# Performance work log

Measured on AMD Instinct MI355X. Metric: run time of the kernel, lower is better.

The kernel has to match this reference:

```python
import jax, jax.numpy as jnp
import numpy as np

B, W, H, C = 8, 32, 32, 64   # batch, width, height, hidden_size (per-head dim)
NH = 8                        # num_attention_heads
P = 64                        # position_encoding_size
M = 32                        # max_position_embeddings
AH = C * NH                   # all_head_size


def setup_inputs() -> dict:
    key = jax.random.key(0)
    ks = jax.random.split(key, 10)
    s = 0.02
    return {
        "hidden_states": jax.random.normal(ks[0], (B, W, H, C), jnp.float32),
        "attention_mask": jnp.zeros((B, W, H), jnp.float32),  # unused by forward (kept for signature parity)
        "row_emb": jax.random.normal(ks[1], (2 * M - 1, P), jnp.float32) * s,
        "col_emb": jax.random.normal(ks[2], (2 * M - 1, P), jnp.float32) * s,
        "w_row": jax.random.normal(ks[3], (NH, P), jnp.float32) * s,  # head_keys_row.weight (no bias)
        "w_col": jax.random.normal(ks[4], (NH, P), jnp.float32) * s,  # head_keys_col.weight (no bias)
        "w_q": jax.random.normal(ks[5], (AH, C), jnp.float32) * s,
        "b_q": jnp.zeros((AH,), jnp.float32),
        "w_k": jax.random.normal(ks[6], (AH, C), jnp.float32) * s,
        "b_k": jnp.zeros((AH,), jnp.float32),
        "w_v": jax.random.normal(ks[7], (C, AH), jnp.float32) * s,  # value: Linear(all_head_size, hidden_size)
        "b_v": jnp.zeros((C,), jnp.float32),
    }


def reference(hidden_states, attention_mask, row_emb, col_emb, w_row, w_col,
              w_q, b_q, w_k, b_k, w_v, b_v):
    b, w, h, c = hidden_states.shape
    nh = w_row.shape[0]
    # relative index table (buffer)
    rel = (jnp.arange(M)[None, :] - jnp.arange(M)[:, None]) + (M - 1)  # (M, M)

    # positional scores
    ri_w = rel[:w, :w].reshape(-1)                                   # (w*w,)
    row_scores = (row_emb[ri_w] @ w_row.T).reshape(1, w, 1, w, nh)   # axis pattern: j,l
    ri_h = rel[:h, :h].reshape(-1)
    col_scores = (col_emb[ri_h] @ w_col.T).reshape(h, 1, h, 1, nh)   # axis pattern: i,k
    pos = (row_scores + col_scores).transpose(0, 1, 4, 2, 3)         # (h, w, nh, h, w)

    # data-dependent scores (use_attention_data=True)
    q = (hidden_states @ w_q.T + b_q).reshape(b, w, h, nh, c)
    k = (hidden_states @ w_k.T + b_k).reshape(b, w, h, nh, c)
    data = jnp.einsum('bijhd,bklhd->bijhkl', q, k) / jnp.sqrt(jnp.float32(c))

    scores = pos[None] + data                                        # (b, w, h, nh, w, h)  (w==h)
    probs = jax.nn.softmax(scores.reshape(b, h, w, nh, h * w), axis=-1)
    probs = probs.reshape(b, h, w, nh, h, w)

    out = jnp.einsum('bijhkl,bkld->bijhd', probs, hidden_states)     # (b, w, h, nh, c)
    out = out.reshape(b, w, h, nh * c)
    return out @ w_v.T + b_v
```

## Files before the change

kernel.cpp:

```cpp
#include <hip/hip_runtime.h>
#include <hip/hip_bf16.h>
#include <cstdint>
#include <cstddef>

#define SB 8
#define SNH 8
#define SS 1024
#define SC 64

typedef __attribute__((ext_vector_type(8)))  short bf16x8;
typedef __attribute__((ext_vector_type(4)))  short bf16x4;
typedef __attribute__((ext_vector_type(4)))  float f32x4;
typedef __attribute__((ext_vector_type(16))) float f32x16;
typedef __attribute__((ext_vector_type(4)))  unsigned u32x4;

#define INVLN2 1.44269504088896f
#define QSCALE (0.125f * INVLN2)

static __device__ __forceinline__ short f2bf(float f) {
    __hip_bfloat16 h = __float2bfloat16(f);
    return __builtin_bit_cast(short, h);
}
static __device__ __forceinline__ float bf2f(short s) {
    return __builtin_bit_cast(float, (unsigned)((unsigned short)s) << 16);
}

static __device__ __forceinline__ bf16x8 cvt8(const float* __restrict__ p, float scl) {
    const float4 a = *(const float4*)p;
    const float4 b = *(const float4*)(p + 4);
    bf16x8 o;
    o[0] = f2bf(a.x * scl); o[1] = f2bf(a.y * scl); o[2] = f2bf(a.z * scl); o[3] = f2bf(a.w * scl);
    o[4] = f2bf(b.x * scl); o[5] = f2bf(b.y * scl); o[6] = f2bf(b.z * scl); o[7] = f2bf(b.w * scl);
    return o;
}
static __device__ __forceinline__ bf16x8 cvt8v(float4 a, float4 b) {
    bf16x8 o;
    o[0] = f2bf(a.x); o[1] = f2bf(a.y); o[2] = f2bf(a.z); o[3] = f2bf(a.w);
    o[4] = f2bf(b.x); o[5] = f2bf(b.y); o[6] = f2bf(b.z); o[7] = f2bf(b.w);
    return o;
}

static __device__ __forceinline__ unsigned pk2(float lo, float hi) {
    return (unsigned)(unsigned short)f2bf(lo) | ((unsigned)(unsigned short)f2bf(hi) << 16);
}

#if __has_builtin(__builtin_amdgcn_permlane32_swap)
typedef __attribute__((ext_vector_type(2))) unsigned uint2v;
static __device__ __forceinline__ void plswap(unsigned& a, unsigned& b) {
    uint2v r = __builtin_amdgcn_permlane32_swap(a, b, false, false);
    a = r[0]; b = r[1];
}
#else
static __device__ __forceinline__ void plswap(unsigned& a, unsigned& b) {
    asm volatile("v_permlane32_swap_b32 %0, %1" : "+v"(a), "+v"(b));
}
#endif

static __device__ __forceinline__ float xhalf_sum(float x) {
    unsigned a = __builtin_bit_cast(unsigned, x), b = a;
    plswap(a, b);
    return __builtin_bit_cast(float, a) + __builtin_bit_cast(float, b);
}

#define MFMA32(a, b, c) __builtin_amdgcn_mfma_f32_32x32x16_bf16((a), (b), (c), 0, 0, 0)

static __device__ __forceinline__ void dlayout_to_bfrag(const float* src, bf16x8* dst) {
#pragma unroll
    for (int k = 0; k < 4; ++k) {
        const int base = (k >> 1) * 16 + (k & 1) * 8;
        unsigned w0 = pk2(src[base + 0], src[base + 1]);
        unsigned w2 = pk2(src[base + 4], src[base + 5]);
        plswap(w0, w2);
        unsigned w1 = pk2(src[base + 2], src[base + 3]);
        unsigned w3 = pk2(src[base + 6], src[base + 7]);
        plswap(w1, w3);
        u32x4 uw; uw[0] = w0; uw[1] = w1; uw[2] = w2; uw[3] = w3;
        dst[k] = __builtin_bit_cast(bf16x8, uw);
    }
}

static __device__ __forceinline__ void dhalf_to_bfrag(const float* src, bf16x8* dst) {
#pragma unroll
    for (int k = 0; k < 2; ++k) {
        const int base = k * 8;
        unsigned w0 = pk2(src[base + 0], src[base + 1]);
        unsigned w2 = pk2(src[base + 4], src[base + 5]);
        plswap(w0, w2);
        unsigned w1 = pk2(src[base + 2], src[base + 3]);
        unsigned w3 = pk2(src[base + 6], src[base + 7]);
        plswap(w1, w3);
        u32x4 uw; uw[0] = w0; uw[1] = w1; uw[2] = w2; uw[3] = w3;
        dst[k] = __builtin_bit_cast(bf16x8, uw);
    }
}

__global__ __launch_bounds__(256) void prep1(
    const float* __restrict__ row_emb, const float* __restrict__ col_emb,
    const float* __restrict__ w_row,   const float* __restrict__ w_col,
    const float* __restrict__ w_v,  const float* __restrict__ w_q,
    const float* __restrict__ w_k,  const float* __restrict__ hid,
    const float* __restrict__ b_q,  const float* __restrict__ b_k,
    float* __restrict__ posRow, float* __restrict__ posCol,
    short* __restrict__ wvB, short* __restrict__ hidB, short* __restrict__ VtBw,
    short* __restrict__ MqBt, float* __restrict__ row0,
    float* __restrict__ vn, float* __restrict__ snv)
{
    const int bx = blockIdx.x;
    const int tid = threadIdx.x;
    __shared__ float T[64][65];

    if (bx < 64) {
        const int idx = bx * 256 + tid;
        const int which = idx >> 13;
        const int r = idx & 8191;
        const int n = r >> 10;
        const int j = (r >> 5) & 31;
        const int l = r & 31;
        const float* emb = which ? col_emb : row_emb;
        const float* wgt = which ? w_col : w_row;
        const int e = l - j + 31;
        float acc = 0.f;
        for (int p = 0; p < 64; p += 4) {
            const float4 ev = *(const float4*)&emb[e * 64 + p];
            const float4 wv4 = *(const float4*)&wgt[n * 64 + p];
            acc += ev.x * wv4.x + ev.y * wv4.y + ev.z * wv4.z + ev.w * wv4.w;
        }
        (which ? posCol : posRow)[r] = acc * INVLN2;
    } else if (bx < 80) {
        const int t = (bx - 64) * 256 + tid;
        *(bf16x8*)&wvB[t * 8] = cvt8(&w_v[t * 8], 1.0f);
    } else if (bx < 208) {
        const int z = bx - 80;
        const int b = z & 7, kt = z >> 3;
        const int r  = tid >> 2;
        const int c0 = (tid & 3) * 16;
        const float* src = hid + (((size_t)b * 1024) + kt * 64 + r) * 64 + c0;
        const float4 f0 = ((const float4*)src)[0];
        const float4 f1 = ((const float4*)src)[1];
        const float4 f2 = ((const float4*)src)[2];
        const float4 f3 = ((const float4*)src)[3];
        T[r][c0 + 0] = f0.x; T[r][c0 + 1] = f0.y; T[r][c0 + 2] = f0.z; T[r][c0 + 3] = f0.w;
        T[r][c0 + 4] = f1.x; T[r][c0 + 5] = f1.y; T[r][c0 + 6] = f1.z; T[r][c0 + 7] = f1.w;
        T[r][c0 + 8] = f2.x; T[r][c0 + 9] = f2.y; T[r][c0 +10] = f2.z; T[r][c0 +11] = f2.w;
        T[r][c0 +12] = f3.x; T[r][c0 +13] = f3.y; T[r][c0 +14] = f3.z; T[r][c0 +15] = f3.w;
        short* hb = hidB + (((size_t)b * 1024) + kt * 64 + r) * 64 + c0;
        *(bf16x8*)(hb)     = cvt8v(f0, f1);
        *(bf16x8*)(hb + 8) = cvt8v(f2, f3);
        __syncthreads();
        short* tbase = VtBw + ((size_t)(b * 16 + kt)) * 4096;
#pragma unroll
        for (int it = 0; it < 2; ++it) {
            const int d  = (tid >> 3) + 32 * it;
            const int k0 = (tid & 7) * 8;
            bf16x8 o;
#pragma unroll
            for (int j = 0; j < 8; ++j) o[j] = f2bf(T[k0 + j][d]);
            *(bf16x8*)&tbase[d * 64 + k0] = o;
        }
    } else {
        const int n = bx - 208;
        const int wv = tid >> 6;
        const int lane = tid & 63;
        if (wv == 0) {
            const int h = lane >> 5, qc = lane & 31;
            bf16x8 afr[2][4], bfr[2][4];
#pragma unroll
            for (int ct = 0; ct < 2; ++ct)
#pragma unroll
                for (int k = 0; k < 4; ++k) {
                    bf16x8 oa, ob;
#pragma unroll
                    for (int j = 0; j < 8; ++j) {
                        const int a = 16 * k + 8 * h + j;
                        oa[j] = f2bf(w_q[(size_t)(n * 64 + a) * 64 + 32 * ct + qc] * QSCALE);
                        ob[j] = f2bf(w_k[(size_t)(n * 64 + a) * 64 + 32 * ct + qc]);
                    }
                    afr[ct][k] = oa; bfr[ct][k] = ob;
                }
#pragma unroll
            for (int ct1 = 0; ct1 < 2; ++ct1)
#pragma unroll
                for (int ctc = 0; ctc < 2; ++ctc) {
                    f32x16 d;
#pragma unroll
                    for (int i = 0; i < 16; ++i) d[i] = 0.f;
                    d = MFMA32(afr[ct1][0], bfr[ctc][0], d);
                    d = MFMA32(afr[ct1][1], bfr[ctc][1], d);
                    d = MFMA32(afr[ct1][2], bfr[ctc][2], d);
                    d = MFMA32(afr[ct1][3], bfr[ctc][3], d);
                    short* mb = MqBt + n * 4096 + (32 * ctc + qc) * 64 + 32 * ct1 + 4 * h;
#pragma unroll
                    for (int rg = 0; rg < 4; ++rg) {
                        bf16x4 ov;
                        ov[0] = f2bf(d[4 * rg + 0]); ov[1] = f2bf(d[4 * rg + 1]);
                        ov[2] = f2bf(d[4 * rg + 2]); ov[3] = f2bf(d[4 * rg + 3]);
                        *(bf16x4*)&mb[8 * rg] = ov;
                    }
                }
        } else if (wv == 1) {
            const int c2 = lane;
            float acc = 0.f;
            for (int a = 0; a < 64; ++a)
                acc += b_q[n * 64 + a] * w_k[(size_t)(n * 64 + a) * 64 + c2];
            row0[n * 64 + c2] = acc * QSCALE;
        } else if (wv == 2) {
            const int c1 = lane;
            float acc = 0.f;
            for (int a = 0; a < 64; ++a)
                acc += b_k[n * 64 + a] * w_q[(size_t)(n * 64 + a) * 64 + c1];
            vn[n * 64 + c1] = acc * QSCALE;
        } else {
            float p = b_q[n * 64 + lane] * b_k[n * 64 + lane];
#pragma unroll
            for (int o = 1; o < 64; o <<= 1) p += __shfl_xor(p, o);
            if (lane == 0) snv[n] = p * QSCALE;
        }
    }
}

__global__ __launch_bounds__(512, 1) void attn_fused(
    const short* __restrict__ hidB, const short* __restrict__ VtBw,
    const short* __restrict__ MqBt, const float* __restrict__ row0,
    const float* __restrict__ vn,   const float* __restrict__ snv,
    const float* __restrict__ posRow, const float* __restrict__ posCol,
    const short* __restrict__ wvB, const float* __restrict__ bv,
    float* __restrict__ out)
{
    const int orig = blockIdx.x;
    const int swzb = (orig & 7) * 32 + (orig >> 3);
    const int b    = swzb >> 5;
    const int qt   = swzb & 31;

    const int tid  = threadIdx.x;
    const int w    = tid >> 6;
    const int n    = w;
    const int lane = tid & 63;
    const int h    = lane >> 5;
    const int qc   = lane & 31;
    const int q    = qt * 32 + qc;
    const int swz  = qc & 7;

    __shared__ __align__(16) short lds[32768];
    short* const Kst0 = lds;
    short* const Vst0 = lds + 4096;
    short* const Kst1 = lds + 8192;
    short* const Vst1 = lds + 12288;

    bf16x8 qf[4];
    float cq;
    {
        const short* hrow = hidB + (((size_t)b * 1024) + q) * 64 + 8 * h;
        bf16x8 hq[4];
#pragma unroll
        for (int kk = 0; kk < 4; ++kk) hq[kk] = *(const bf16x8*)(hrow + 16 * kk);

        float aD[32];
#pragma unroll
        for (int ct = 0; ct < 2; ++ct) {
            f32x16 ci;
            const float* r0p = row0 + n * 64 + 32 * ct + 4 * h;
#pragma unroll
            for (int rg = 0; rg < 4; ++rg) {
                const float4 v = *(const float4*)(r0p + 8 * rg);
                ci[4 * rg + 0] = v.x; ci[4 * rg + 1] = v.y;
                ci[4 * rg + 2] = v.z; ci[4 * rg + 3] = v.w;
            }
            const short* mbase = MqBt + n * 4096 + (size_t)(32 * ct + qc) * 64 + 8 * h;
            ci = MFMA32(*(const bf16x8*)(mbase),      hq[0], ci);
            ci = MFMA32(*(const bf16x8*)(mbase + 16), hq[1], ci);
            ci = MFMA32(*(const bf16x8*)(mbase + 32), hq[2], ci);
            ci = MFMA32(*(const bf16x8*)(mbase + 48), hq[3], ci);
#pragma unroll
            for (int i = 0; i < 16; ++i) aD[16 * ct + i] = ci[i];
        }
        dlayout_to_bfrag(aD, qf);

        float part = 0.f;
#pragma unroll
        for (int kk = 0; kk < 4; ++kk) {
            const float4 v0 = *(const float4*)&vn[n * 64 + 16 * kk + 8 * h];
            const float4 v1 = *(const float4*)&vn[n * 64 + 16 * kk + 8 * h + 4];
            part += bf2f(hq[kk][0]) * v0.x + bf2f(hq[kk][1]) * v0.y +
                    bf2f(hq[kk][2]) * v0.z + bf2f(hq[kk][3]) * v0.w +
                    bf2f(hq[kk][4]) * v1.x + bf2f(hq[kk][5]) * v1.y +
                    bf2f(hq[kk][6]) * v1.z + bf2f(hq[kk][7]) * v1.w;
        }
        cq = xhalf_sum(part) + snv[n];
    }

    float prowA[16];
    {
        const float* pr = posRow + (n * 32 + qc) * 32 + 4 * h;
#pragma unroll
        for (int rg = 0; rg < 4; ++rg) {
            const float4 v = *(const float4*)(pr + 8 * rg);
            prowA[4 * rg + 0] = v.x + cq; prowA[4 * rg + 1] = v.y + cq;
            prowA[4 * rg + 2] = v.z + cq; prowA[4 * rg + 3] = v.w + cq;
        }
    }
    const float* pcp = posCol + (n * 32 + qt) * 32;

    const short* Kbase = hidB + (size_t)b * 65536;
    const short* Vbase = VtBw + (size_t)b * 65536;

    const int c16  = tid & 7;
    const int srow = tid >> 3;
    const int woff = srow * 128 + ((c16 ^ (srow & 7)) << 4);
    const short* kp = Kbase + (size_t)srow * 64 + c16 * 8;
    const short* vp = Vbase + (size_t)srow * 64 + c16 * 8;

    float lsum = 0.f;
    f32x16 oacc[2];
#pragma unroll
    for (int dt = 0; dt < 2; ++dt)
#pragma unroll
        for (int i = 0; i < 16; ++i) oacc[dt][i] = 0.f;

    auto compute = [&](int kt, const short* Ktc_s, const short* Vtc_s) {
        const char* Ktc = (const char*)Ktc_s;
        const char* Vtc = (const char*)Vtc_s;
        const float pcv[2] = {pcp[2 * kt], pcp[2 * kt + 1]};

        bf16x8 pfrag[4];
#pragma unroll
        for (int ct = 0; ct < 2; ++ct) {
            bf16x8 kf[4];
            const int rb = (32 * ct + qc) * 128;
#pragma unroll
            for (int k = 0; k < 4; ++k)
                kf[k] = *(const bf16x8*)(Ktc + rb + (((2 * k + h) ^ swz) << 4));

            f32x16 ci;
#pragma unroll
            for (int i = 0; i < 16; ++i) ci[i] = prowA[i] + pcv[ct];
            ci = MFMA32(kf[0], qf[0], ci);
            ci = MFMA32(kf[1], qf[1], ci);
            ci = MFMA32(kf[2], qf[2], ci);
            ci = MFMA32(kf[3], qf[3], ci);

            float p[16];
#pragma unroll
            for (int i = 0; i < 16; ++i) p[i] = __builtin_amdgcn_exp2f(ci[i]);
            float s8[8];
#pragma unroll
            for (int i = 0; i < 8; ++i) s8[i] = p[i] + p[i + 8];
            lsum += ((s8[0] + s8[1]) + (s8[2] + s8[3])) +
                    ((s8[4] + s8[5]) + (s8[6] + s8[7]));
            dhalf_to_bfrag(p, &pfrag[2 * ct]);
        }

        bf16x8 vf[2][4];
#pragma unroll
        for (int dt = 0; dt < 2; ++dt) {
            const int rb = (32 * dt + qc) * 128;
#pragma unroll
            for (int ks = 0; ks < 4; ++ks)
                vf[dt][ks] = *(const bf16x8*)(Vtc + rb + (((2 * ks + h) ^ swz) << 4));
        }
#pragma unroll
        for (int dt = 0; dt < 2; ++dt) {
            f32x16 oa = oacc[dt];
            oa = MFMA32(vf[dt][0], pfrag[0], oa);
            oa = MFMA32(vf[dt][1], pfrag[1], oa);
            oa = MFMA32(vf[dt][2], pfrag[2], oa);
            oacc[dt] = MFMA32(vf[dt][3], pfrag[3], oa);
        }
    };

    {
        const float4 a0 = *(const float4*)kp;
        const float4 a1 = *(const float4*)vp;
        *(float4*)((char*)Kst0 + woff) = a0;
        *(float4*)((char*)Vst0 + woff) = a1;
    }
    __syncthreads();

#pragma unroll 1
    for (int pr = 0; pr < 8; ++pr) {
        const int j0 = 2 * pr, j1 = j0 + 1;
        {
            const size_t o = (size_t)(j0 + 1) * 4096;
            const float4 a0 = *(const float4*)(kp + o);
            const float4 a1 = *(const float4*)(vp + o);
            compute(j0, Kst0, Vst0);
            *(float4*)((char*)Kst1 + woff) = a0;
            *(float4*)((char*)Vst1 + woff) = a1;
            __syncthreads();
        }
        if (j1 < 15) {
            const size_t o = (size_t)(j1 + 1) * 4096;
            const float4 a0 = *(const float4*)(kp + o);
            const float4 a1 = *(const float4*)(vp + o);
            compute(j1, Kst1, Vst1);
            *(float4*)((char*)Kst0 + woff) = a0;
            *(float4*)((char*)Vst0 + woff) = a1;
            __syncthreads();
        } else {
            compute(j1, Kst1, Vst1);
        }
    }

    const float inv = 1.0f / xhalf_sum(lsum);
    float hoD[32];
#pragma unroll
    for (int dt = 0; dt < 2; ++dt)
#pragma unroll
        for (int i = 0; i < 16; ++i) hoD[16 * dt + i] = oacc[dt][i] * inv;
    bf16x8 hofrag[4];
    dlayout_to_bfrag(hoD, hofrag);

    f32x16 dvacc[2];
#pragma unroll
    for (int ct = 0; ct < 2; ++ct)
#pragma unroll
        for (int i = 0; i < 16; ++i) dvacc[ct][i] = 0.f;
#pragma unroll
    for (int ct = 0; ct < 2; ++ct)
#pragma unroll
        for (int k = 0; k < 4; ++k) {
            const bf16x8 aw = *(const bf16x8*)&wvB[(size_t)(32 * ct + qc) * 512 +
                                                   n * 64 + 16 * k + 8 * h];
            dvacc[ct] = MFMA32(aw, hofrag[k], dvacc[ct]);
        }

    __syncthreads();
    float* cb = (float*)lds;
#pragma unroll
    for (int i = 0; i < 32; ++i)
        cb[n * 2048 + i * 64 + lane] = dvacc[i >> 4][i & 15];
    __syncthreads();

    float s[4];
#pragma unroll
    for (int k = 0; k < 4; ++k) {
        const int i = 4 * w + k;
        float acc = 0.f;
#pragma unroll
        for (int nn = 0; nn < 8; ++nn) acc += cb[nn * 2048 + i * 64 + lane];
        s[k] = acc;
    }
    const int dvb = 32 * (w >> 2) + 8 * (w & 3) + 4 * h;
    const float4 bb4 = *(const float4*)&bv[dvb];
    const int row = b * 1024 + qt * 32 + qc;
    *(float4*)&out[(size_t)row * 64 + dvb] =
        make_float4(s[0] + bb4.x, s[1] + bb4.y, s[2] + bb4.z, s[3] + bb4.w);
}

extern "C" void kernel_launch(void* const* d_in, const int* in_sizes, int n_in,
                              void* d_out, int out_size, void* d_ws, size_t ws_size,
                              hipStream_t stream)
{
    const float* hid     = (const float*)d_in[0];
    const float* row_emb = (const float*)d_in[2];
    const float* col_emb = (const float*)d_in[3];
    const float* w_row   = (const float*)d_in[4];
    const float* w_col   = (const float*)d_in[5];
    const float* w_q     = (const float*)d_in[6];
    const float* b_q     = (const float*)d_in[7];
    const float* w_k     = (const float*)d_in[8];
    const float* b_k     = (const float*)d_in[9];
    const float* w_v     = (const float*)d_in[10];
    const float* b_v     = (const float*)d_in[11];
    float* out = (float*)d_out;

    short* hidB   = (short*)d_ws;
    short* VtBw   = hidB + (size_t)SB * SS * SC;
    short* MqBt   = VtBw + (size_t)SB * SS * SC;
    float* posRow = (float*)(MqBt + SNH * SC * SC);
    float* posCol = posRow + SNH * 32 * 32;
    float* row0   = posCol + SNH * 32 * 32;
    float* vn     = row0 + SNH * SC;
    float* snv    = vn + SNH * SC;
    short* wvB    = (short*)(snv + 8);

    prep1<<<216, 256, 0, stream>>>(row_emb, col_emb, w_row, w_col, w_v, w_q,
                                   w_k, hid, b_q, b_k,
                                   posRow, posCol, wvB, hidB, VtBw,
                                   MqBt, row0, vn, snv);
    attn_fused<<<256, 512, 0, stream>>>(hidB, VtBw, MqBt, row0, vn, snv,
                                        posRow, posCol, wvB, b_v, out);
}
```

Measured before the change: 39.57 us.

## Split heads across two blocks and combine output projection with atomics

The attention kernel now launches 512 blocks of 256 threads, each handling four heads for one query tile, instead of 256 blocks of 512 threads covering all eight heads. The aim is more blocks and occupancy (two blocks per CU) on the GPU's many compute units. Each block reduces its four heads' partial value projections in shared memory and atomically adds them into the output. The prep kernel gains extra blocks that pre-initialise the output with the bias. This costs float atomics, output results that depend on the order of those atomics, and K/V tiles that are loaded twice per query tile.

```diff
diff --git a/kernel.cpp b/kernel.cpp
--- a/kernel.cpp
+++ b/kernel.cpp
@@ -100,10 +100,12 @@
     const float* __restrict__ w_v,  const float* __restrict__ w_q,
     const float* __restrict__ w_k,  const float* __restrict__ hid,
     const float* __restrict__ b_q,  const float* __restrict__ b_k,
+    const float* __restrict__ b_v,
     float* __restrict__ posRow, float* __restrict__ posCol,
     short* __restrict__ wvB, short* __restrict__ hidB, short* __restrict__ VtBw,
     short* __restrict__ MqBt, float* __restrict__ row0,
-    float* __restrict__ vn, float* __restrict__ snv)
+    float* __restrict__ vn, float* __restrict__ snv,
+    float* __restrict__ out)
 {
     const int bx = blockIdx.x;
     const int tid = threadIdx.x;
@@ -157,7 +159,7 @@
             for (int j = 0; j < 8; ++j) o[j] = f2bf(T[k0 + j][d]);
             *(bf16x8*)&tbase[d * 64 + k0] = o;
         }
-    } else {
+    } else if (bx < 216) {
         const int n = bx - 208;
         const int wv = tid >> 6;
         const int lane = tid & 63;
@@ -215,32 +217,45 @@
             for (int o = 1; o < 64; o <<= 1) p += __shfl_xor(p, o);
             if (lane == 0) snv[n] = p * QSCALE;
         }
-    }
-}
-
-__global__ __launch_bounds__(512, 1) void attn_fused(
+    } else {
+        const int t = (bx - 216) * 256 + tid;
+        float4 bvv[16];
+#pragma unroll
+        for (int i = 0; i < 16; ++i) bvv[i] = *(const float4*)&b_v[i * 4];
+#pragma unroll
+        for (int r = 0; r < 4; ++r) {
+            float* op = out + ((size_t)t * 4 + r) * 64;
+#pragma unroll
+            for (int i = 0; i < 16; ++i) *(float4*)&op[i * 4] = bvv[i];
+        }
+    }
+}
+
+__global__ __launch_bounds__(256, 2) void attn_fused(
     const short* __restrict__ hidB, const short* __restrict__ VtBw,
     const short* __restrict__ MqBt, const float* __restrict__ row0,
     const float* __restrict__ vn,   const float* __restrict__ snv,
     const float* __restrict__ posRow, const float* __restrict__ posCol,
-    const short* __restrict__ wvB, const float* __restrict__ bv,
+    const short* __restrict__ wvB,
     float* __restrict__ out)
 {
     const int orig = blockIdx.x;
-    const int swzb = (orig & 7) * 32 + (orig >> 3);
-    const int b    = swzb >> 5;
-    const int qt   = swzb & 31;
+    const int swzb = (orig & 7) * 64 + (orig >> 3);
+    const int b    = swzb >> 6;
+    const int rest = swzb & 63;
+    const int qt   = rest >> 1;
+    const int g    = rest & 1;
 
     const int tid  = threadIdx.x;
     const int w    = tid >> 6;
-    const int n    = w;
+    const int n    = g * 4 + w;
     const int lane = tid & 63;
     const int h    = lane >> 5;
     const int qc   = lane & 31;
     const int q    = qt * 32 + qc;
     const int swz  = qc & 7;
 
-    __shared__ __align__(16) short lds[32768];
+    __shared__ __align__(16) short lds[16384];
     short* const Kst0 = lds;
     short* const Vst0 = lds + 4096;
     short* const Kst1 = lds + 8192;
@@ -305,9 +320,12 @@
 
     const int c16  = tid & 7;
     const int srow = tid >> 3;
-    const int woff = srow * 128 + ((c16 ^ (srow & 7)) << 4);
-    const short* kp = Kbase + (size_t)srow * 64 + c16 * 8;
-    const short* vp = Vbase + (size_t)srow * 64 + c16 * 8;
+    const int woffA = srow * 128 + ((c16 ^ (srow & 7)) << 4);
+    const int woffB = (srow + 32) * 128 + ((c16 ^ (srow & 7)) << 4);
+    const short* kp0 = Kbase + (size_t)srow * 64 + c16 * 8;
+    const short* kp1 = Kbase + (size_t)(srow + 32) * 64 + c16 * 8;
+    const short* vp0 = Vbase + (size_t)srow * 64 + c16 * 8;
+    const short* vp1 = Vbase + (size_t)(srow + 32) * 64 + c16 * 8;
 
     float lsum = 0.f;
     f32x16 oacc[2];
@@ -368,35 +386,47 @@
     };
 
     {
-        const float4 a0 = *(const float4*)kp;
-        const float4 a1 = *(const float4*)vp;
-        *(float4*)((char*)Kst0 + woff) = a0;
-        *(float4*)((char*)Vst0 + woff) = a1;
+        const float4 a0 = *(const float4*)kp0;
+        const float4 a1 = *(const float4*)kp1;
+        const float4 a2 = *(const float4*)vp0;
+        const float4 a3 = *(const float4*)vp1;
+        *(float4*)((char*)Kst0 + woffA) = a0;
+        *(float4*)((char*)Kst0 + woffB) = a1;
+        *(float4*)((char*)Vst0 + woffA) = a2;
+        *(float4*)((char*)Vst0 + woffB) = a3;
     }
     __syncthreads();
 
 #pragma unroll 1
     for (int pr = 0; pr < 8; ++pr) {
-        const int j0 = 2 * pr, j1 = j0 + 1;
+        const int kt0 = 2 * pr, kt1 = kt0 + 1;
         {
-            const size_t o = (size_t)(j0 + 1) * 4096;
-            const float4 a0 = *(const float4*)(kp + o);
-            const float4 a1 = *(const float4*)(vp + o);
-            compute(j0, Kst0, Vst0);
-            *(float4*)((char*)Kst1 + woff) = a0;
-            *(float4*)((char*)Vst1 + woff) = a1;
+            const size_t o = (size_t)(kt0 + 1) * 4096;
+            const float4 a0 = *(const float4*)(kp0 + o);
+            const float4 a1 = *(const float4*)(kp1 + o);
+            const float4 a2 = *(const float4*)(vp0 + o);
+            const float4 a3 = *(const float4*)(vp1 + o);
+            compute(kt0, Kst0, Vst0);
+            *(float4*)((char*)Kst1 + woffA) = a0;
+            *(float4*)((char*)Kst1 + woffB) = a1;
+            *(float4*)((char*)Vst1 + woffA) = a2;
+            *(float4*)((char*)Vst1 + woffB) = a3;
             __syncthreads();
         }
-        if (j1 < 15) {
-            const size_t o = (size_t)(j1 + 1) * 4096;
-            const float4 a0 = *(const float4*)(kp + o);
-            const float4 a1 = *(const float4*)(vp + o);
-            compute(j1, Kst1, Vst1);
-            *(float4*)((char*)Kst0 + woff) = a0;
-            *(float4*)((char*)Vst0 + woff) = a1;
+        if (kt1 < 15) {
+            const size_t o = (size_t)(kt1 + 1) * 4096;
+            const float4 a0 = *(const float4*)(kp0 + o);
+            const float4 a1 = *(const float4*)(kp1 + o);
+            const float4 a2 = *(const float4*)(vp0 + o);
+            const float4 a3 = *(const float4*)(vp1 + o);
+            compute(kt1, Kst1, Vst1);
+            *(float4*)((char*)Kst0 + woffA) = a0;
+            *(float4*)((char*)Kst0 + woffB) = a1;
+            *(float4*)((char*)Vst0 + woffA) = a2;
+            *(float4*)((char*)Vst0 + woffB) = a3;
             __syncthreads();
         } else {
-            compute(j1, Kst1, Vst1);
+            compute(kt1, Kst1, Vst1);
         }
     }
 
@@ -427,23 +457,20 @@
     float* cb = (float*)lds;
 #pragma unroll
     for (int i = 0; i < 32; ++i)
-        cb[n * 2048 + i * 64 + lane] = dvacc[i >> 4][i & 15];
+        cb[w * 2048 + i * 64 + lane] = dvacc[i >> 4][i & 15];
     __syncthreads();
 
-    float s[4];
-#pragma unroll
-    for (int k = 0; k < 4; ++k) {
-        const int i = 4 * w + k;
-        float acc = 0.f;
-#pragma unroll
-        for (int nn = 0; nn < 8; ++nn) acc += cb[nn * 2048 + i * 64 + lane];
-        s[k] = acc;
-    }
-    const int dvb = 32 * (w >> 2) + 8 * (w & 3) + 4 * h;
-    const float4 bb4 = *(const float4*)&bv[dvb];
     const int row = b * 1024 + qt * 32 + qc;
-    *(float4*)&out[(size_t)row * 64 + dvb] =
-        make_float4(s[0] + bb4.x, s[1] + bb4.y, s[2] + bb4.z, s[3] + bb4.w);
+    float* orow = out + (size_t)row * 64;
+#pragma unroll
+    for (int k = 0; k < 8; ++k) {
+        const int i = 8 * w + k;
+        float acc = cb[i * 64 + lane];
+#pragma unroll
+        for (int nn = 1; nn < 4; ++nn) acc += cb[nn * 2048 + i * 64 + lane];
+        const int dv = 32 * (i >> 4) + 8 * ((i >> 2) & 3) + 4 * h + (i & 3);
+        atomicAdd(&orow[dv], acc);
+    }
 }
 
 extern "C" void kernel_launch(void* const* d_in, const int* in_sizes, int n_in,
@@ -473,10 +500,10 @@
     float* snv    = vn + SNH * SC;
     short* wvB    = (short*)(snv + 8);
 
-    prep1<<<216, 256, 0, stream>>>(row_emb, col_emb, w_row, w_col, w_v, w_q,
-                                   w_k, hid, b_q, b_k,
+    prep1<<<224, 256, 0, stream>>>(row_emb, col_emb, w_row, w_col, w_v, w_q,
+                                   w_k, hid, b_q, b_k, b_v,
                                    posRow, posCol, wvB, hidB, VtBw,
-                                   MqBt, row0, vn, snv);
-    attn_fused<<<256, 512, 0, stream>>>(hidB, VtBw, MqBt, row0, vn, snv,
-                                        posRow, posCol, wvB, b_v, out);
-}
+                                   MqBt, row0, vn, snv, out);
+    attn_fused<<<512, 256, 0, stream>>>(hidB, VtBw, MqBt, row0, vn, snv,
+                                        posRow, posCol, wvB, out);
+}
```

After: 66.29 us. 67.5% more time.
